# Performance work log

Measured on AMD Instinct MI355X. Metric: run time of the kernel, lower is better.

The kernel has to match this reference:

```python
import jax, jax.numpy as jnp
import numpy as np
from jax import lax

STRIDE, PADDING, DILATION = 1, 1, 1


def setup_inputs() -> dict:
    key = jax.random.key(0)
    ks = jax.random.split(key, 6)
    B, C, H, W = 32, 128, 64, 64
    K, O, ksz = 4, 256, 3
    red = 32  # C // reduction
    # kaiming-ish scales
    return {
        "x": jax.random.normal(ks[0], (B, C, H, W), jnp.float32),
        "weights": jax.random.normal(ks[1], (K, O, C, ksz, ksz), jnp.float32) * (1.0 / np.sqrt(C * ksz * ksz)),
        "w1": jax.random.normal(ks[2], (red, C), jnp.float32) * (1.0 / np.sqrt(C)),
        "b1": jnp.zeros((red,), jnp.float32),
        "w2": jax.random.normal(ks[3], (K, red), jnp.float32) * (1.0 / np.sqrt(red)),
        "b2": jnp.zeros((K,), jnp.float32),
    }


def reference(x, weights, w1, b1, w2, b2):
    B, C, H, W = x.shape
    K, O, Cw, kh, kw = weights.shape
    # attention over kernels: global avg pool -> MLP -> softmax  [B, K]
    pooled = jnp.mean(x, axis=(2, 3))                       # [B, C]
    h = jax.nn.relu(pooled @ w1.T + b1)                     # [B, red]
    att = jax.nn.softmax(h @ w2.T + b2, axis=1)             # [B, K]
    # per-sample mixed kernel: [B, O, C, kh, kw]
    wk = jnp.einsum('bk,koihw->boihw', att, weights)
    # batched per-sample conv via grouped convolution (groups = B)
    lhs = x.reshape(1, B * C, H, W)
    rhs = wk.reshape(B * O, C, kh, kw)
    out = lax.conv_general_dilated(
        lhs, rhs,
        window_strides=(STRIDE, STRIDE),
        padding=[(PADDING, PADDING), (PADDING, PADDING)],
        rhs_dilation=(DILATION, DILATION),
        dimension_numbers=('NCHW', 'OIHW', 'NCHW'),
        feature_group_count=B,
    )
    Ho, Wo = out.shape[2], out.shape[3]
    return out.reshape(B, O, Ho, Wo)
```

## Files before the change

### kernel.cpp

```cpp
#include <hip/hip_runtime.h>
#include <math.h>

#define BB 32
#define CC 128
#define HH 64
#define WW 64
#define KK 4
#define OO 256
#define RED 32
#define HWSZ (HH*WW)
#define XT_W 66
#define GPLANE (XT_W*XT_W)

typedef __attribute__((ext_vector_type(8))) short bf16x8;
typedef __attribute__((ext_vector_type(4))) float f32x4;
typedef __attribute__((ext_vector_type(16))) float f32x16;

static __device__ __forceinline__ unsigned short f2bf(float f) {
    unsigned int u = __float_as_uint(f);
    u += 0x7FFF + ((u >> 16) & 1);
    return (unsigned short)(u >> 16);
}

static __device__ __forceinline__ void async16(unsigned short* lds, const unsigned short* g) {
    __builtin_amdgcn_global_load_lds(
        (const __attribute__((address_space(1))) unsigned int*)g,
        (__attribute__((address_space(3))) unsigned int*)lds, 16, 0, 0);
}

__global__ __launch_bounds__(256) void transpose_pool(const float* __restrict__ x,
        unsigned short* __restrict__ xt, float* __restrict__ partial) {
    __shared__ float lt[CC][65];
    int h = blockIdx.x & 63;
    int b = blockIdx.x >> 6;
    const float* xb = x + ((size_t)b * CC * HH + h) * WW;
    for (int i = threadIdx.x; i < CC * 16; i += 256) {
        int c = i >> 4, f4 = i & 15;
        float4 v = *(const float4*)(xb + (size_t)c * HWSZ + f4 * 4);
        lt[c][f4 * 4 + 0] = v.x;
        lt[c][f4 * 4 + 1] = v.y;
        lt[c][f4 * 4 + 2] = v.z;
        lt[c][f4 * 4 + 3] = v.w;
    }
    __syncthreads();
    size_t bg = (size_t)b * 4;
    for (int i = threadIdx.x; i < 64 * 16; i += 256) {
        int ww = i >> 4, cs = i & 15;
        bf16x8 pk;
#pragma unroll
        for (int j = 0; j < 8; ++j) pk[j] = (short)f2bf(lt[cs * 8 + j][ww]);
        *(bf16x8*)&xt[(((bg + (cs >> 2)) * XT_W + (h + 1)) * XT_W + (ww + 1)) * 32 + (cs & 3) * 8] = pk;
    }
    if (threadIdx.x < 32) {
        int cs = threadIdx.x & 15;
        int col = (threadIdx.x < 16) ? 0 : 65;
        *(f32x4*)&xt[(((bg + (cs >> 2)) * XT_W + (h + 1)) * XT_W + col) * 32 + (cs & 3) * 8] =
            (f32x4){0.f, 0.f, 0.f, 0.f};
    }
    if (h == 0 || h == 63) {
        int hr = (h == 0) ? 0 : 65;
        for (int i = threadIdx.x; i < XT_W * 16; i += 256) {
            int px = i >> 4, cs = i & 15;
            *(f32x4*)&xt[(((bg + (cs >> 2)) * XT_W + hr) * XT_W + px) * 32 + (cs & 3) * 8] =
                (f32x4){0.f, 0.f, 0.f, 0.f};
        }
    }
    if (threadIdx.x < CC) {
        float s = 0.f;
#pragma unroll
        for (int j = 0; j < WW; ++j) s += lt[threadIdx.x][j];
        partial[(size_t)blockIdx.x * CC + threadIdx.x] = s;
    }
}

__global__ void att_kernel(const float* __restrict__ partial,
        const float* __restrict__ w1, const float* __restrict__ b1,
        const float* __restrict__ w2, const float* __restrict__ b2,
        float* __restrict__ att) {
    int b = blockIdx.x;
    int tid = threadIdx.x;
    __shared__ float ps[CC];
    __shared__ float hs[RED];
    __shared__ float ls[KK];
    if (tid < CC) {
        const float* pp = partial + (size_t)b * HH * CC + tid;
        float s = 0.f;
#pragma unroll
        for (int h = 0; h < HH; ++h) s += pp[(size_t)h * CC];
        ps[tid] = s * (1.0f / (float)HWSZ);
    }
    __syncthreads();
    int r = tid >> 3, j = tid & 7;
    const float* w1r = w1 + r * CC + j * 16;
    float p = 0.f;
#pragma unroll
    for (int c = 0; c < 16; ++c) p = fmaf(ps[j * 16 + c], w1r[c], p);
    p += __shfl_xor(p, 1, 64);
    p += __shfl_xor(p, 2, 64);
    p += __shfl_xor(p, 4, 64);
    if (j == 0) hs[r] = fmaxf(p + b1[r], 0.f);
    __syncthreads();
    if (tid < KK) {
        float acc = b2[tid];
        const float* w2k = w2 + tid * RED;
#pragma unroll
        for (int rr = 0; rr < RED; ++rr) acc = fmaf(hs[rr], w2k[rr], acc);
        ls[tid] = acc;
    }
    __syncthreads();
    if (tid == 0) {
        float m = fmaxf(fmaxf(ls[0], ls[1]), fmaxf(ls[2], ls[3]));
        float e0 = expf(ls[0] - m), e1 = expf(ls[1] - m);
        float e2 = expf(ls[2] - m), e3 = expf(ls[3] - m);
        float inv = 1.0f / (e0 + e1 + e2 + e3);
        att[b * KK + 0] = e0 * inv; att[b * KK + 1] = e1 * inv;
        att[b * KK + 2] = e2 * inv; att[b * KK + 3] = e3 * inv;
    }
}

__global__ __launch_bounds__(256) void mix_kernel(const float* __restrict__ w,
        const float* __restrict__ att, unsigned short* __restrict__ wk) {
    int gid = blockIdx.x * 256 + threadIdx.x;
    int c = gid & 127;
    int o = (gid >> 7) & 255;
    int b = gid >> 15;
    float a[KK];
#pragma unroll
    for (int k = 0; k < KK; ++k) a[k] = att[b * KK + k];
    float mixed[9];
#pragma unroll
    for (int t = 0; t < 9; ++t) mixed[t] = 0.f;
#pragma unroll
    for (int k = 0; k < KK; ++k) {
        const float* p = w + (((size_t)k * OO + o) * CC + c) * 9;
#pragma unroll
        for (int t = 0; t < 9; ++t) mixed[t] = fmaf(a[k], p[t], mixed[t]);
    }
    size_t base = ((size_t)b * 4 + (c >> 5)) * 9;
#pragma unroll
    for (int t = 0; t < 9; ++t)
        wk[((base + t) * OO + o) * 32 + (c & 31)] = f2bf(mixed[t]);
}

#define XS_C 32
#define AL_C 32
__global__ __launch_bounds__(256, 2) void conv_mfma(const unsigned short* __restrict__ xt,
        const unsigned short* __restrict__ wk, float* __restrict__ out) {
    __shared__ unsigned short xs[6 * XT_W * XS_C];
    __shared__ unsigned short als[3][128 * AL_C];

    int bid = blockIdx.x;
    int blk = (bid & 7) * 128 + (bid >> 3);
    int b  = blk >> 5;
    int rg = (blk >> 1) & 15;
    int ot = blk & 1;
    int r0 = rg * 4;
    int o0 = ot * 128;

    int tid = threadIdx.x;
    int lane = tid & 63;
    int wid = tid >> 6;
    int wm = wid & 1;
    int wn = wid >> 1;
    int l31 = lane & 31;
    int lh = lane >> 5;

    f32x16 acc[2][4];
#pragma unroll
    for (int i = 0; i < 2; ++i)
#pragma unroll
        for (int j = 0; j < 4; ++j)
#pragma unroll
            for (int r = 0; r < 16; ++r) acc[i][j][r] = 0.f;

    const unsigned short* xt_b = xt + (size_t)b * 4 * GPLANE * 32;
    const unsigned short* wk_b = wk + ((size_t)b * 4 * 9 * OO + o0) * 32;

    for (int g = 0; g < 4; ++g) {
        __syncthreads();
        const unsigned short* xsrc = xt_b + ((size_t)g * GPLANE + r0 * XT_W) * 32;
        for (int i = tid; i < 1584; i += 256) {
            int pix = i >> 2, seg = i & 3;
            int segg = seg ^ ((pix >> 1) & 3);
            async16(xs + i * 8, xsrc + pix * 32 + segg * 8);
        }
        const unsigned short* wsrc = wk_b + (size_t)g * 9 * OO * 32;
        {
            int ch = tid;
#pragma unroll
            for (int rep = 0; rep < 2; ++rep, ch += 256) {
                int o = ch >> 2, seg = ch & 3;
                int segg = seg ^ ((o >> 1) & 3);
                async16(als[0] + ch * 8, wsrc + o * 32 + segg * 8);
            }
        }
        __syncthreads();

#pragma unroll
        for (int t = 0; t < 9; ++t) {
            if (t < 8) {
                int nb = (t + 1) % 3;
                int ch = tid;
#pragma unroll
                for (int rep = 0; rep < 2; ++rep, ch += 256) {
                    int o = ch >> 2, seg = ch & 3;
                    int segg = seg ^ ((o >> 1) & 3);
                    async16(als[nb] + ch * 8,
                            wsrc + ((size_t)(t + 1) * OO + o) * 32 + segg * 8);
                }
                asm volatile("s_waitcnt vmcnt(2)" ::: "memory");
            } else {
                asm volatile("s_waitcnt vmcnt(0)" ::: "memory");
            }
            __builtin_amdgcn_s_barrier();
            asm volatile("" ::: "memory");

            int kh = t / 3, kw = t - kh * 3;
            const unsigned short* alsb = als[t % 3];
            bf16x8 af[2][2], bfv[4][2];
#pragma unroll
            for (int m = 0; m < 2; ++m) {
                int orow = wm * 64 + m * 32 + l31;
#pragma unroll
                for (int kk = 0; kk < 2; ++kk) {
                    int s = kk * 2 + lh;
                    af[m][kk] = *(const bf16x8*)&alsb[orow * AL_C +
                                                     (s ^ ((orow >> 1) & 3)) * 8];
                }
            }
#pragma unroll
            for (int nf = 0; nf < 4; ++nf) {
                int prow = wn * 2 + (nf >> 1) + kh;
                int pcol = (nf & 1) * 32 + l31 + kw;
                int pix = prow * XT_W + pcol;
#pragma unroll
                for (int kk = 0; kk < 2; ++kk) {
                    int s = kk * 2 + lh;
                    bfv[nf][kk] = *(const bf16x8*)&xs[pix * XS_C +
                                                      (s ^ ((pix >> 1) & 3)) * 8];
                }
            }
#pragma unroll
            for (int kk = 0; kk < 2; ++kk)
#pragma unroll
                for (int m = 0; m < 2; ++m)
#pragma unroll
                    for (int nf = 0; nf < 4; ++nf)
                        acc[m][nf] = __builtin_amdgcn_mfma_f32_32x32x16_bf16(
                            af[m][kk], bfv[nf][kk], acc[m][nf], 0, 0, 0);
        }
    }

    float* outb = out + ((size_t)b * OO + o0) * HWSZ;
#pragma unroll
    for (int m = 0; m < 2; ++m)
#pragma unroll
        for (int nf = 0; nf < 4; ++nf) {
            int row = r0 + wn * 2 + (nf >> 1);
            int col = (nf & 1) * 32 + l31;
#pragma unroll
            for (int r = 0; r < 16; ++r) {
                int o = wm * 64 + m * 32 + (r & 3) + 8 * (r >> 2) + 4 * lh;
                __builtin_nontemporal_store(acc[m][nf][r],
                    &outb[(size_t)o * HWSZ + row * WW + col]);
            }
        }
}

extern "C" void kernel_launch(void* const* d_in, const int* in_sizes, int n_in,
                              void* d_out, int out_size, void* d_ws, size_t ws_size,
                              hipStream_t stream) {
    const float* x       = (const float*)d_in[0];
    const float* weights = (const float*)d_in[1];
    const float* w1      = (const float*)d_in[2];
    const float* b1      = (const float*)d_in[3];
    const float* w2      = (const float*)d_in[4];
    const float* b2      = (const float*)d_in[5];
    float* out = (float*)d_out;

    char* ws = (char*)d_ws;
    float* partial      = (float*)ws;
    float* att          = (float*)(ws + 1048576);
    unsigned short* wk  = (unsigned short*)(ws + 1048576 + 4096);
    unsigned short* xtp = (unsigned short*)(ws + 1048576 + 4096 + 18874368);

    transpose_pool<<<BB * HH, 256, 0, stream>>>(x, xtp, partial);
    att_kernel<<<BB, 256, 0, stream>>>(partial, w1, b1, w2, b2, att);
    mix_kernel<<<BB * OO * CC / 256, 256, 0, stream>>>(weights, att, wk);
    conv_mfma<<<BB * 2 * 16, 256, 0, stream>>>(xtp, wk, out);
}
```

Measured before the change: 263.7 us.

## Split channel groups into 8-channel planes to replace XOR swizzle in LDS

Changes the global layout of the transposed input and mixed weights from 32-channel interleaved pixels to separate 8-channel sub-planes. Each LDS tile is stored as four contiguous sub-planes, so MFMA fragment loads index directly without the XOR swizzle. The goal is to remove swizzle address arithmetic and get conflict-free LDS reads from plain consecutive-pixel access. In exchange, the global loads now read 16B chunks from four separate planes, and the transpose kernel's writes are scattered across more planes.

```diff
diff --git a/kernel.cpp b/kernel.cpp
--- a/kernel.cpp
+++ b/kernel.cpp
@@ -43,25 +43,27 @@
         lt[c][f4 * 4 + 3] = v.w;
     }
     __syncthreads();
-    size_t bg = (size_t)b * 4;
-    for (int i = threadIdx.x; i < 64 * 16; i += 256) {
-        int ww = i >> 4, cs = i & 15;
+    for (int i = threadIdx.x; i < 16 * 64; i += 256) {
+        int cs = i >> 6, ww = i & 63;
         bf16x8 pk;
 #pragma unroll
         for (int j = 0; j < 8; ++j) pk[j] = (short)f2bf(lt[cs * 8 + j][ww]);
-        *(bf16x8*)&xt[(((bg + (cs >> 2)) * XT_W + (h + 1)) * XT_W + (ww + 1)) * 32 + (cs & 3) * 8] = pk;
+        size_t plane = ((size_t)b * 4 + (cs >> 2)) * 4 + (cs & 3);
+        *(bf16x8*)&xt[((plane * XT_W + (h + 1)) * XT_W + (ww + 1)) * 8] = pk;
     }
     if (threadIdx.x < 32) {
         int cs = threadIdx.x & 15;
         int col = (threadIdx.x < 16) ? 0 : 65;
-        *(f32x4*)&xt[(((bg + (cs >> 2)) * XT_W + (h + 1)) * XT_W + col) * 32 + (cs & 3) * 8] =
+        size_t plane = ((size_t)b * 4 + (cs >> 2)) * 4 + (cs & 3);
+        *(f32x4*)&xt[((plane * XT_W + (h + 1)) * XT_W + col) * 8] =
             (f32x4){0.f, 0.f, 0.f, 0.f};
     }
     if (h == 0 || h == 63) {
         int hr = (h == 0) ? 0 : 65;
         for (int i = threadIdx.x; i < XT_W * 16; i += 256) {
             int px = i >> 4, cs = i & 15;
-            *(f32x4*)&xt[(((bg + (cs >> 2)) * XT_W + hr) * XT_W + px) * 32 + (cs & 3) * 8] =
+            size_t plane = ((size_t)b * 4 + (cs >> 2)) * 4 + (cs & 3);
+            *(f32x4*)&xt[((plane * XT_W + hr) * XT_W + px) * 8] =
                 (f32x4){0.f, 0.f, 0.f, 0.f};
         }
     }
@@ -136,18 +138,18 @@
 #pragma unroll
         for (int t = 0; t < 9; ++t) mixed[t] = fmaf(a[k], p[t], mixed[t]);
     }
-    size_t base = ((size_t)b * 4 + (c >> 5)) * 9;
+    int g = c >> 5, s = (c >> 3) & 3, j = c & 7;
+    size_t base = ((size_t)b * 4 + g) * 9 * 8192 + ((size_t)s * 256 + o) * 8 + j;
 #pragma unroll
     for (int t = 0; t < 9; ++t)
-        wk[((base + t) * OO + o) * 32 + (c & 31)] = f2bf(mixed[t]);
-}
-
-#define XS_C 32
-#define AL_C 32
+        wk[base + (size_t)t * 8192] = f2bf(mixed[t]);
+}
+
+#define XSP 396
 __global__ __launch_bounds__(256, 2) void conv_mfma(const unsigned short* __restrict__ xt,
         const unsigned short* __restrict__ wk, float* __restrict__ out) {
-    __shared__ unsigned short xs[6 * XT_W * XS_C];
-    __shared__ unsigned short als[3][128 * AL_C];
+    __shared__ unsigned short xs[4 * XSP * 8];
+    __shared__ unsigned short als[3][4 * 128 * 8];
 
     int bid = blockIdx.x;
     int blk = (bid & 7) * 128 + (bid >> 3);
@@ -173,25 +175,24 @@
 #pragma unroll
             for (int r = 0; r < 16; ++r) acc[i][j][r] = 0.f;
 
-    const unsigned short* xt_b = xt + (size_t)b * 4 * GPLANE * 32;
-    const unsigned short* wk_b = wk + ((size_t)b * 4 * 9 * OO + o0) * 32;
+    const unsigned short* xt_b = xt + (size_t)b * 4 * 4 * GPLANE * 8;
+    const unsigned short* wk_b = wk + (size_t)b * 4 * 9 * 8192;
 
     for (int g = 0; g < 4; ++g) {
+        const unsigned short* xsg  = xt_b + (size_t)g * 4 * GPLANE * 8;
+        const unsigned short* wsrc = wk_b + (size_t)g * 9 * 8192;
         __syncthreads();
-        const unsigned short* xsrc = xt_b + ((size_t)g * GPLANE + r0 * XT_W) * 32;
-        for (int i = tid; i < 1584; i += 256) {
-            int pix = i >> 2, seg = i & 3;
-            int segg = seg ^ ((pix >> 1) & 3);
-            async16(xs + i * 8, xsrc + pix * 32 + segg * 8);
-        }
-        const unsigned short* wsrc = wk_b + (size_t)g * 9 * OO * 32;
+        for (int i = tid; i < 4 * XSP; i += 256) {
+            int s = i / XSP, pix = i - s * XSP;
+            async16(xs + (size_t)i * 8,
+                    xsg + ((size_t)s * GPLANE + r0 * XT_W + pix) * 8);
+        }
         {
             int ch = tid;
 #pragma unroll
             for (int rep = 0; rep < 2; ++rep, ch += 256) {
-                int o = ch >> 2, seg = ch & 3;
-                int segg = seg ^ ((o >> 1) & 3);
-                async16(als[0] + ch * 8, wsrc + o * 32 + segg * 8);
+                async16(als[0] + (size_t)ch * 8,
+                        wsrc + ((size_t)(ch >> 7) * 256 + o0 + (ch & 127)) * 8);
             }
         }
         __syncthreads();
@@ -200,13 +201,12 @@
         for (int t = 0; t < 9; ++t) {
             if (t < 8) {
                 int nb = (t + 1) % 3;
+                const unsigned short* tsrc = wsrc + (size_t)(t + 1) * 8192;
                 int ch = tid;
 #pragma unroll
                 for (int rep = 0; rep < 2; ++rep, ch += 256) {
-                    int o = ch >> 2, seg = ch & 3;
-                    int segg = seg ^ ((o >> 1) & 3);
-                    async16(als[nb] + ch * 8,
-                            wsrc + ((size_t)(t + 1) * OO + o) * 32 + segg * 8);
+                    async16(als[nb] + (size_t)ch * 8,
+                            tsrc + ((size_t)(ch >> 7) * 256 + o0 + (ch & 127)) * 8);
                 }
                 asm volatile("s_waitcnt vmcnt(2)" ::: "memory");
             } else {
@@ -224,8 +224,7 @@
 #pragma unroll
                 for (int kk = 0; kk < 2; ++kk) {
                     int s = kk * 2 + lh;
-                    af[m][kk] = *(const bf16x8*)&alsb[orow * AL_C +
-                                                     (s ^ ((orow >> 1) & 3)) * 8];
+                    af[m][kk] = *(const bf16x8*)&alsb[((size_t)s * 128 + orow) * 8];
                 }
             }
 #pragma unroll
@@ -236,8 +235,7 @@
 #pragma unroll
                 for (int kk = 0; kk < 2; ++kk) {
                     int s = kk * 2 + lh;
-                    bfv[nf][kk] = *(const bf16x8*)&xs[pix * XS_C +
-                                                      (s ^ ((pix >> 1) & 3)) * 8];
+                    bfv[nf][kk] = *(const bf16x8*)&xs[((size_t)s * XSP + pix) * 8];
                 }
             }
 #pragma unroll
```

Result: no change. 267.1 us (median of 2 runs) (+1.3%).
